# Kernel tuning notes

Measured on AMD Instinct MI355X. Metric: run time of the kernel, lower is better.

Reference implementation:

```python
import jax, jax.numpy as jnp
import numpy as np

V, E, H, F, A, L = 32000, 256, 512, 512, 256, 49  # vocab, embed, hidden, feature, attn, n_locations
B, T = 64, 32


def setup_inputs() -> dict:
    key = jax.random.key(0)
    ks = jax.random.split(key, 16)
    s = lambda k, sh: (jax.random.normal(k, sh, jnp.float32) * 0.02)
    embedding = s(ks[0], (V, E)).at[0].set(0.0)  # padding_idx=0 row zeroed
    return dict(
        image_feats=jax.random.normal(ks[1], (B, L, F), jnp.float32),
        caption_in=jax.random.randint(ks[2], (B, T), 0, V, dtype=jnp.int32),
        embedding=embedding,
        W_init_h=s(ks[3], (F, H)), b_init_h=jnp.zeros((H,), jnp.float32),
        W_init_c=s(ks[4], (F, H)), b_init_c=jnp.zeros((H,), jnp.float32),
        W_feat=s(ks[5], (F, A)), b_feat=jnp.zeros((A,), jnp.float32),
        W_hid=s(ks[6], (H, A)), b_hid=jnp.zeros((A,), jnp.float32),
        W_score=s(ks[7], (A,)), b_score=jnp.zeros((), jnp.float32),
        W_ih=s(ks[8], (E + F, 4 * H)), b_ih=jnp.zeros((4 * H,), jnp.float32),
        W_hh=s(ks[9], (H, 4 * H)), b_hh=jnp.zeros((4 * H,), jnp.float32),
        W_out=s(ks[10], (H, V)), b_out=jnp.zeros((V,), jnp.float32),
    )


def reference(image_feats, caption_in, embedding,
              W_init_h, b_init_h, W_init_c, b_init_c,
              W_feat, b_feat, W_hid, b_hid, W_score, b_score,
              W_ih, b_ih, W_hh, b_hh, W_out, b_out):
    # init_hidden_state: mean over spatial locations -> two linears
    mean_feats = image_feats.mean(axis=1)                      # (B, F)
    h0 = mean_feats @ W_init_h + b_init_h                      # (B, H)
    c0 = mean_feats @ W_init_c + b_init_c                      # (B, H)
    embs = embedding[caption_in]                               # (B, T, E); dropout = identity (eval)
    feat_proj = image_feats @ W_feat + b_feat                  # (B, L, A) - invariant over t, precompute

    def step(carry, emb_t):
        h, c = carry
        # additive attention
        energy = jnp.tanh(feat_proj + (h @ W_hid + b_hid)[:, None, :])   # (B, L, A)
        scores = energy @ W_score + b_score                              # (B, L)
        alpha = jax.nn.softmax(scores, axis=1)                           # (B, L)
        context = jnp.einsum('bl,blf->bf', alpha, image_feats)           # (B, F)
        # LSTMCell (torch gate order i, f, g, o)
        x = jnp.concatenate([emb_t, context], axis=1)                    # (B, E+F)
        gates = x @ W_ih + b_ih + h @ W_hh + b_hh                        # (B, 4H)
        i, f, g, o = jnp.split(gates, 4, axis=1)
        i = jax.nn.sigmoid(i); f = jax.nn.sigmoid(f); o = jax.nn.sigmoid(o)
        c_new = f * c + i * jnp.tanh(g)
        h_new = o * jnp.tanh(c_new)
        logits_t = h_new @ W_out + b_out                                 # (B, V); dropout = identity
        return (h_new, c_new), (logits_t, alpha)

    _, (logits, alphas) = jax.lax.scan(step, (h0, c0), jnp.swapaxes(embs, 0, 1))
    predictions = jnp.swapaxes(logits, 0, 1)   # (B, T, V)
    all_alphas = jnp.swapaxes(alphas, 0, 1)    # (B, T, L)
    return predictions, all_alphas
```

## Files before the change

kernel.cpp:

```cpp
#include <hip/hip_runtime.h>
#include <hip/hip_bf16.h>

typedef _Float16 f16;
typedef _Float16 f16x8 __attribute__((ext_vector_type(8)));
typedef _Float16 f16x4 __attribute__((ext_vector_type(4)));
typedef _Float16 f16x2 __attribute__((ext_vector_type(2)));
typedef float f32x4 __attribute__((ext_vector_type(4)));
typedef unsigned long long ull;

#define B_ 64
#define T_ 32
#define L_ 49
#define F_ 512
#define H_ 512
#define A_ 256
#define E_ 256
#define V_ 32000
#define G4 2048
#define NG 32
#define NLOG 125
#define SLOT 16

#define ALOAD32(p)     __hip_atomic_load((const unsigned*)(p), __ATOMIC_RELAXED, __HIP_MEMORY_SCOPE_AGENT)
#define ASTORE32(p, v) __hip_atomic_store((unsigned*)(p), (v), __ATOMIC_RELAXED, __HIP_MEMORY_SCOPE_AGENT)
#define ASTORE64(p, v) __hip_atomic_store((ull*)(p), (v), __ATOMIC_RELAXED, __HIP_MEMORY_SCOPE_AGENT)
#define AADD(p)        __hip_atomic_fetch_add((unsigned*)(p), 1u, __ATOMIC_RELAXED, __HIP_MEMORY_SCOPE_AGENT)

#if defined(__has_builtin)
#if __has_builtin(__builtin_amdgcn_fdot2)
#define HAS_FDOT2 1
#endif
#endif

#define NB_TC0 (64 * 24)
#define NB_TC1 (64 * 16)
#define NB_TC2 (1000 * 16)
#define NB_TC3 (8 * 16)
#define NB_CVT 1568
#define NB_EMB 2048
#define NB_INIT 64
#define NB_FP  196

__device__ void dev_tcvt(const float* __restrict__ x, f16* __restrict__ y,
                         int R, int C, int bx, int by, char* smem) {
    float (*ls)[33] = (float(*)[33])smem;
    int c0 = bx * 32, r0 = by * 32;
    int tid = threadIdx.x;
    int rr = tid >> 3, cs = (tid & 7) * 4;
    float4 v = *(const float4*)&x[(size_t)(r0 + rr) * C + c0 + cs];
    ls[rr][cs] = v.x; ls[rr][cs + 1] = v.y; ls[rr][cs + 2] = v.z; ls[rr][cs + 3] = v.w;
    __syncthreads();
    int cr = tid >> 3, rs = (tid & 7) * 4;
    f16x4 o = {(f16)ls[rs][cr], (f16)ls[rs + 1][cr], (f16)ls[rs + 2][cr], (f16)ls[rs + 3][cr]};
    *(f16x4*)&y[(size_t)(c0 + cr) * R + r0 + rs] = o;
}

__global__ __launch_bounds__(256) void k_prep(
    const float* __restrict__ image_feats, const int* __restrict__ caption,
    const float* __restrict__ embedding,
    const float* __restrict__ W_init_h, const float* __restrict__ b_init_h,
    const float* __restrict__ W_init_c, const float* __restrict__ b_init_c,
    const float* __restrict__ W_feat, const float* __restrict__ b_feat,
    const float* __restrict__ W_hid, const float* __restrict__ W_ih,
    const float* __restrict__ W_hh, const float* __restrict__ W_out,
    f16* __restrict__ feats16, f16* __restrict__ embs16,
    f16* __restrict__ WihT, f16* __restrict__ WhhT,
    f16* __restrict__ WoutT, f16* __restrict__ WhidT,
    f16* __restrict__ hslab, float* __restrict__ c_cur,
    float* __restrict__ featproj) {
    __shared__ __align__(16) char smem[32768];
    int bid = blockIdx.x, tid = threadIdx.x;
    int r = bid;
    if (r < NB_TC0) { dev_tcvt(W_ih, WihT, E_ + F_, G4, r % 64, r / 64, smem); return; }
    r -= NB_TC0;
    if (r < NB_TC1) { dev_tcvt(W_hh, WhhT, H_, G4, r % 64, r / 64, smem); return; }
    r -= NB_TC1;
    if (r < NB_TC2) { dev_tcvt(W_out, WoutT, H_, V_, r % 1000, r / 1000, smem); return; }
    r -= NB_TC2;
    if (r < NB_TC3) { dev_tcvt(W_hid, WhidT, H_, A_, r % 8, r / 8, smem); return; }
    r -= NB_TC3;
    if (r < NB_CVT) {
        int i = r * 256 + tid;
        float4 v = ((const float4*)image_feats)[i];
        f16x4 h = {(f16)v.x, (f16)v.y, (f16)v.z, (f16)v.w};
        ((f16x4*)feats16)[i] = h;
        return;
    }
    r -= NB_CVT;
    if (r < NB_EMB) {
        int tok = caption[r];
        embs16[(size_t)r * E_ + tid] = (f16)embedding[(size_t)tok * E_ + tid];
        return;
    }
    r -= NB_EMB;
    if (r < NB_INIT) {
        float* mean = (float*)smem;
        int b = r;
        for (int f = tid; f < F_; f += 256) {
            float s = 0.f;
            for (int l = 0; l < L_; ++l) s += image_feats[((size_t)b * L_ + l) * F_ + f];
            mean[f] = s * (1.f / 49.f);
        }
        __syncthreads();
        for (int h = tid; h < H_; h += 256) {
            float a = b_init_h[h], c = b_init_c[h];
            for (int k = 0; k < F_; ++k) {
                float m = mean[k];
                a += m * W_init_h[k * H_ + h];
                c += m * W_init_c[k * H_ + h];
            }
            hslab[(size_t)b * H_ + h] = (f16)a;
            c_cur[b * H_ + h] = c;
        }
        return;
    }
    r -= NB_INIT;
    {
        float (*fs)[F_] = (float(*)[F_])smem;
        int r0 = r * 16;
        for (int i = tid; i < 16 * F_; i += 256)
            fs[i >> 9][i & 511] = image_feats[(size_t)r0 * F_ + i];
        __syncthreads();
        float acc[16];
#pragma unroll
        for (int q = 0; q < 16; ++q) acc[q] = 0.f;
        for (int k = 0; k < F_; ++k) {
            float w = W_feat[k * A_ + tid];
#pragma unroll
            for (int q = 0; q < 16; ++q) acc[q] += fs[q][k] * w;
        }
        float bb = b_feat[tid];
#pragma unroll
        for (int q = 0; q < 16; ++q) featproj[(size_t)(r0 + q) * A_ + tid] = acc[q] + bb;
    }
}

struct Smem128 { f16 As[128][40]; f16 Bs[128][40]; };

__device__ __forceinline__ void gemm128_body1(
    const f16* __restrict__ A, int lda, const f16* __restrict__ Bt, int ldb,
    f16* __restrict__ Cv, int M, int K, int mtiles, int bid,
    const float* __restrict__ bias0, const float* __restrict__ bias1, Smem128* sm) {
    int m0 = (bid % mtiles) * 128, n0 = (bid / mtiles) * 128;
    int tid = threadIdx.x, lane = tid & 63, wave = tid >> 6;
    int wr = (wave >> 1) * 64, wc = (wave & 1) * 64;
    int frow = lane & 15, fk = (lane >> 4) * 8;
    int ra = tid >> 2, ka = (tid & 3) * 8;
    f32x4 acc[4][4];
#pragma unroll
    for (int i = 0; i < 4; ++i)
#pragma unroll
        for (int j = 0; j < 4; ++j) { acc[i][j][0]=0.f; acc[i][j][1]=0.f; acc[i][j][2]=0.f; acc[i][j][3]=0.f; }

    for (int k0 = 0; k0 < K; k0 += 32) {
        f16x8 a0 = *(const f16x8*)&A[(size_t)(m0 + ra) * lda + k0 + ka];
        f16x8 a1 = *(const f16x8*)&A[(size_t)(m0 + 64 + ra) * lda + k0 + ka];
        f16x8 b0 = *(const f16x8*)&Bt[(size_t)(n0 + ra) * ldb + k0 + ka];
        f16x8 b1 = *(const f16x8*)&Bt[(size_t)(n0 + 64 + ra) * ldb + k0 + ka];
        __syncthreads();
        *(f16x8*)&sm->As[ra][ka] = a0;
        *(f16x8*)&sm->As[64 + ra][ka] = a1;
        *(f16x8*)&sm->Bs[ra][ka] = b0;
        *(f16x8*)&sm->Bs[64 + ra][ka] = b1;
        __syncthreads();
        f16x8 av[4], bv[4];
#pragma unroll
        for (int i = 0; i < 4; ++i) {
            av[i] = *(f16x8*)&sm->As[wr + i * 16 + frow][fk];
            bv[i] = *(f16x8*)&sm->Bs[wc + i * 16 + frow][fk];
        }
#pragma unroll
        for (int mi = 0; mi < 4; ++mi)
#pragma unroll
            for (int ni = 0; ni < 4; ++ni)
                acc[mi][ni] = __builtin_amdgcn_mfma_f32_16x16x32_f16(av[mi], bv[ni], acc[mi][ni], 0, 0, 0);
    }
    int rq = (lane >> 4) * 4;
#pragma unroll
    for (int mi = 0; mi < 4; ++mi)
#pragma unroll
        for (int ni = 0; ni < 4; ++ni) {
            int cc = n0 + wc + ni * 16 + frow;
            float badd = (bias0 ? bias0[cc] : 0.f) + (bias1 ? bias1[cc] : 0.f);
#pragma unroll
            for (int r = 0; r < 4; ++r) {
                int rr = m0 + wr + mi * 16 + rq + r;
                if (rr < M)
                    Cv[((size_t)rr * 512 + (cc & 511)) * 4 + (cc >> 9)] =
                        (f16)(acc[mi][ni][r] + badd);
            }
        }
}

__global__ __launch_bounds__(256) void k_gemm_pre(
    int split,
    const f16* A0, int lda0, const f16* B0, int ldb0, f16* C0, int M0, int K0, int mt0,
    const f16* A1, int lda1, const f16* B1, int ldb1, f16* C1, int M1, int K1, int mt1,
    const float* bias0, const float* bias1) {
    __shared__ Smem128 sm;
    int bid = blockIdx.x;
    if (bid < split)
        gemm128_body1(A0, lda0, B0, ldb0, C0, M0, K0, mt0, bid,
                      (const float*)nullptr, (const float*)nullptr, &sm);
    else
        gemm128_body1(A1, lda1, B1, ldb1, C1, M1, K1, mt1, bid - split,
                      bias0, bias1, &sm);
}

struct GateSm {
    float fp[L_][A_];
    float ea[A_];
    float ws[A_];
    float sc[64];
    float alpha[64];
    unsigned hL[256];
};
struct GemmSm {
    f16 w[64][512];
    union {
        f16 hs[64][512];
        f16 hwT16[64][72];
    } u;
};
struct LogSm { f16 hs[64][512]; };

__device__ __forceinline__ void wait_cnt(const unsigned* p, unsigned target) {
    if (threadIdx.x == 0) {
        while (ALOAD32(p) < target) __builtin_amdgcn_s_sleep(1);
    }
    __syncthreads();
    asm volatile("" ::: "memory");
}

__device__ __forceinline__ float sigm(float x) { return 1.f / (1.f + __expf(-x)); }
__device__ __forceinline__ float tanh_f(float x) { return 1.f - 2.f / (1.f + __expf(2.f * x)); }

__global__ __launch_bounds__(256, 1) void k_steps(
    const f16* __restrict__ WhhT, const f16* __restrict__ WhidT,
    const float* __restrict__ featproj, const float* __restrict__ b_hid,
    const float* __restrict__ W_score, const float* __restrict__ b_score,
    const f16* __restrict__ embP, const f16* __restrict__ fp2P,
    const float* __restrict__ c_cur,
    f16* __restrict__ hslab, f16* __restrict__ hwslab,
    const f16* __restrict__ WoutT, const float* __restrict__ b_out,
    float* __restrict__ preds, float* __restrict__ out_alpha,
    unsigned* __restrict__ cntH, unsigned* __restrict__ cntW,
    unsigned* __restrict__ cntH2) {
    __shared__ __align__(16) char smraw[sizeof(GemmSm)];
    int bid = blockIdx.x, tid = threadIdx.x;

    if (bid < 64) {
        int b = bid;
        GateSm* S = (GateSm*)smraw;
        for (int i = tid; i < L_ * A_; i += 256)
            ((float*)S->fp)[i] = featproj[(size_t)b * L_ * A_ + i];
        S->ws[tid] = W_score[tid];
        float bhid_r = b_hid[tid];
        float bsc = b_score[0];
        S->hL[tid] = ((const unsigned*)hslab)[(size_t)b * 256 + tid];
        float cs0 = c_cur[b * H_ + 2 * tid], cs1 = c_cur[b * H_ + 2 * tid + 1];
        const f16* wrow = WhidT + (size_t)tid * 512;
        int wv = tid >> 6, ln = tid & 63;
        __syncthreads();

        for (int t = 0; t < T_; ++t) {
            {
                float acc = bhid_r;
                const f16x8* hL8 = (const f16x8*)S->hL;
#pragma unroll 16
                for (int kk = 0; kk < 64; ++kk) {
                    union { f16x8 v; f16x2 p[4]; } uw, uh;
                    uw.v = *(const f16x8*)&wrow[kk * 8];
                    uh.v = hL8[kk];
#ifdef HAS_FDOT2
                    acc = __builtin_amdgcn_fdot2(uw.p[0], uh.p[0], acc, false);
                    acc = __builtin_amdgcn_fdot2(uw.p[1], uh.p[1], acc, false);
                    acc = __builtin_amdgcn_fdot2(uw.p[2], uh.p[2], acc, false);
                    acc = __builtin_amdgcn_fdot2(uw.p[3], uh.p[3], acc, false);
#else
#pragma unroll
                    for (int e = 0; e < 8; ++e) acc += (float)uw.v[e] * (float)uh.v[e];
#endif
                }
                S->ea[tid] = acc;
            }
            __syncthreads();
            for (int l = wv; l < L_; l += 4) {
                float p = 0.f;
#pragma unroll
                for (int q = 0; q < 4; ++q) {
                    int j = ln + q * 64;
                    p += tanh_f(S->fp[l][j] + S->ea[j]) * S->ws[j];
                }
#pragma unroll
                for (int off = 32; off > 0; off >>= 1) p += __shfl_xor(p, off);
                if (ln == 0) S->sc[l] = p;
            }
            __syncthreads();
            if (tid < 64) {
                float v = (tid < L_) ? S->sc[tid] + bsc : -3.4e38f;
                float m = v;
#pragma unroll
                for (int off = 32; off > 0; off >>= 1) m = fmaxf(m, __shfl_xor(m, off));
                float e = (tid < L_) ? __expf(v - m) : 0.f;
                float s = e;
#pragma unroll
                for (int off = 32; off > 0; off >>= 1) s += __shfl_xor(s, off);
                if (tid < L_) {
                    float al = e / s;
                    S->alpha[tid] = al;
                    out_alpha[((size_t)b * T_ + t) * L_ + tid] = al;
                }
            }
            __syncthreads();
            float s8[8];
#pragma unroll
            for (int i = 0; i < 8; ++i) s8[i] = 0.f;
            {
                const f16* fpb = fp2P + (size_t)b * L_ * G4 + 8 * tid;
#pragma unroll 7
                for (int l = 0; l < L_; ++l) {
                    float a = S->alpha[l];
                    f16x8 fv = *(const f16x8*)&fpb[(size_t)l * G4];
#pragma unroll
                    for (int i = 0; i < 8; ++i) s8[i] += a * (float)fv[i];
                }
            }
            f16x8 ep = *(const f16x8*)&embP[((size_t)b * T_ + t) * G4 + 8 * tid];
            wait_cnt(&cntW[t * SLOT], NG);
            {
                f16x8 hw = *(const f16x8*)&hwslab[((size_t)t * B_ + b) * G4 + 8 * tid];
                float gA[8];
#pragma unroll
                for (int i = 0; i < 8; ++i) gA[i] = (float)hw[i] + (float)ep[i] + s8[i];
                float cn0 = sigm(gA[1]) * cs0 + sigm(gA[0]) * tanh_f(gA[2]);
                float cn1 = sigm(gA[5]) * cs1 + sigm(gA[4]) * tanh_f(gA[6]);
                float hn0 = sigm(gA[3]) * tanh_f(cn0);
                float hn1 = sigm(gA[7]) * tanh_f(cn1);
                cs0 = cn0; cs1 = cn1;
                union { f16 h[2]; unsigned u; } pk;
                pk.h[0] = (f16)hn0; pk.h[1] = (f16)hn1;
                S->hL[tid] = pk.u;
                ASTORE32((unsigned*)hslab + ((size_t)(t + 1) * B_ + b) * 256 + tid, pk.u);
            }
            __syncthreads();
            if (tid == 0) {
                AADD(&cntH[(t + 1) * SLOT]);
                AADD(&cntH2[(t + 1) * SLOT]);
            }
        }
    } else if (bid < 64 + NG) {
        int g = bid - 64;
        GemmSm* S = (GemmSm*)smraw;
        for (int i = 0; i < 16; ++i) {
            int idx = i * 256 + tid;
            int r = idx >> 6, ch = idx & 63;
            int cc = (r & 3) * 512 + 16 * g + (r >> 2);
            *(f16x8*)&S->w[r][(ch ^ (r & 7)) * 8] =
                *(const f16x8*)&WhhT[(size_t)cc * 512 + ch * 8];
        }
        int wvv = tid >> 6, lane = tid & 63;
        int frow = lane & 15, q = lane >> 4, sw = frow & 7, rq = q * 4;
        int bo = tid >> 2, cq = (tid & 3) * 4;
        __syncthreads();

        for (int t = 0; t < T_; ++t) {
            if (t) wait_cnt(&cntH[t * SLOT], 64);
            {
                const f16* hsrc = hslab + (size_t)t * B_ * H_;
#pragma unroll
                for (int i = 0; i < 16; ++i) {
                    int idx = i * 256 + tid;
                    int r = idx >> 6, ch = idx & 63;
                    *(f16x8*)&S->u.hs[r][(ch ^ (r & 7)) * 8] =
                        *(const f16x8*)&hsrc[(size_t)r * H_ + ch * 8];
                }
            }
            __syncthreads();
            f32x4 a4[4];
#pragma unroll
            for (int mi = 0; mi < 4; ++mi) { a4[mi][0]=0.f; a4[mi][1]=0.f; a4[mi][2]=0.f; a4[mi][3]=0.f; }
#pragma unroll
            for (int kk = 0; kk < 16; ++kk) {
                int ch = ((kk * 4 + q) ^ sw) * 8;
                f16x8 bv = *(f16x8*)&S->w[wvv * 16 + frow][ch];
#pragma unroll
                for (int mi = 0; mi < 4; ++mi) {
                    f16x8 av = *(f16x8*)&S->u.hs[mi * 16 + frow][ch];
                    a4[mi] = __builtin_amdgcn_mfma_f32_16x16x32_f16(av, bv, a4[mi], 0, 0, 0);
                }
            }
            __syncthreads();
#pragma unroll
            for (int mi = 0; mi < 4; ++mi)
#pragma unroll
                for (int r = 0; r < 4; ++r)
                    S->u.hwT16[mi * 16 + rq + r][wvv * 16 + frow] = (f16)a4[mi][r];
            __syncthreads();
            {
                f16* dst = hwslab + ((size_t)t * B_ + bo) * G4 + 64 * g + cq;
#pragma unroll
                for (int e = 0; e < 4; ++e) {
                    union { f16 h[4]; ull u; } pk;
                    *(f16x4*)pk.h = *(f16x4*)&S->u.hwT16[bo][cq + 16 * e];
                    ASTORE64(dst + 16 * e, pk.u);
                }
            }
            __syncthreads();
            if (tid == 0) AADD(&cntW[t * SLOT]);
        }
    } else {
        int nt = bid - 64 - NG;
        int n0 = nt * 256;
        LogSm* S = (LogSm*)smraw;
        int wvv = tid >> 6, lane = tid & 63;
        int frow = lane & 15, q = lane >> 4, sw = frow & 7, rq = q * 4;

        for (int t = 0; t < T_; ++t) {
            wait_cnt(&cntH2[(t + 1) * SLOT], 64);
            {
                const f16* hsrc = hslab + (size_t)(t + 1) * B_ * H_;
#pragma unroll
                for (int i = 0; i < 16; ++i) {
                    int idx = i * 256 + tid;
                    int r = idx >> 6, ch = idx & 63;
                    *(f16x8*)&S->hs[r][(ch ^ (r & 7)) * 8] =
                        *(const f16x8*)&hsrc[(size_t)r * H_ + ch * 8];
                }
            }
            __syncthreads();
            f32x4 acc[4][4];
#pragma unroll
            for (int mi = 0; mi < 4; ++mi)
#pragma unroll
                for (int ni = 0; ni < 4; ++ni) { acc[mi][ni][0]=0.f; acc[mi][ni][1]=0.f; acc[mi][ni][2]=0.f; acc[mi][ni][3]=0.f; }
#pragma unroll 4
            for (int kk = 0; kk < 16; ++kk) {
                int ch = ((kk * 4 + q) ^ sw) * 8;
                f16x8 av[4], bv[4];
#pragma unroll
                for (int mi = 0; mi < 4; ++mi)
                    av[mi] = *(f16x8*)&S->hs[mi * 16 + frow][ch];
#pragma unroll
                for (int ni = 0; ni < 4; ++ni)
                    bv[ni] = *(const f16x8*)&WoutT[(size_t)(n0 + wvv * 64 + ni * 16 + frow) * 512 + kk * 32 + q * 8];
#pragma unroll
                for (int mi = 0; mi < 4; ++mi)
#pragma unroll
                    for (int ni = 0; ni < 4; ++ni)
                        acc[mi][ni] = __builtin_amdgcn_mfma_f32_16x16x32_f16(av[mi], bv[ni], acc[mi][ni], 0, 0, 0);
            }
#pragma unroll
            for (int ni = 0; ni < 4; ++ni) {
                int cc = n0 + wvv * 64 + ni * 16 + frow;
                float badd = b_out[cc];
#pragma unroll
                for (int mi = 0; mi < 4; ++mi)
#pragma unroll
                    for (int r = 0; r < 4; ++r) {
                        int b = mi * 16 + rq + r;
                        preds[((size_t)b * T_ + t) * V_ + cc] = acc[mi][ni][r] + badd;
                    }
            }
        }
    }
}

extern "C" void kernel_launch(void* const* d_in, const int* in_sizes, int n_in,
                              void* d_out, int out_size, void* d_ws, size_t ws_size,
                              hipStream_t stream) {
    const float* image_feats = (const float*)d_in[0];
    const int*   caption     = (const int*)d_in[1];
    const float* embedding   = (const float*)d_in[2];
    const float* W_init_h    = (const float*)d_in[3];
    const float* b_init_h    = (const float*)d_in[4];
    const float* W_init_c    = (const float*)d_in[5];
    const float* b_init_c    = (const float*)d_in[6];
    const float* W_feat      = (const float*)d_in[7];
    const float* b_feat      = (const float*)d_in[8];
    const float* W_hid       = (const float*)d_in[9];
    const float* b_hid       = (const float*)d_in[10];
    const float* W_score     = (const float*)d_in[11];
    const float* b_score     = (const float*)d_in[12];
    const float* W_ih        = (const float*)d_in[13];
    const float* b_ih        = (const float*)d_in[14];
    const float* W_hh        = (const float*)d_in[15];
    const float* b_hh        = (const float*)d_in[16];
    const float* W_out       = (const float*)d_in[17];
    const float* b_out       = (const float*)d_in[18];

    float* preds = (float*)d_out;
    float* out_alpha = preds + (size_t)B_ * T_ * V_;

    size_t off = 0;
    char* base = (char*)d_ws;
    auto carve = [&](size_t bytes) {
        void* p = base + off;
        off += (bytes + 255) & ~(size_t)255;
        return p;
    };
    const int MP = 3200;
    f16* fp2P       = (f16*)carve((size_t)MP * G4 * 2);
    f16* embP       = (f16*)carve((size_t)B_ * T_ * G4 * 2);
    float* featproj = (float*)carve((size_t)B_ * L_ * A_ * 4);
    float* c_cur    = (float*)carve((size_t)B_ * H_ * 4);
    f16* hslab      = (f16*)carve((size_t)(T_ + 1) * B_ * H_ * 2);
    f16* hwslab     = (f16*)carve((size_t)T_ * B_ * G4 * 2);
    unsigned* cnts  = (unsigned*)carve(3 * (T_ + 2) * SLOT * 4);
    f16* feats16    = (f16*)carve((size_t)MP * F_ * 2);
    f16* embs16     = (f16*)carve((size_t)B_ * T_ * E_ * 2);
    f16* WihT       = (f16*)carve((size_t)G4 * (E_ + F_) * 2);
    f16* WhhT       = (f16*)carve((size_t)G4 * H_ * 2);
    f16* WoutT      = (f16*)carve((size_t)V_ * H_ * 2);
    f16* WhidT      = (f16*)carve((size_t)A_ * H_ * 2);
    unsigned* cntH  = cnts;
    unsigned* cntW  = cnts + (T_ + 2) * SLOT;
    unsigned* cntH2 = cnts + 2 * (T_ + 2) * SLOT;
    (void)ws_size; (void)in_sizes; (void)n_in; (void)out_size;

    {
        int nb = NB_TC0 + NB_TC1 + NB_TC2 + NB_TC3 + NB_CVT + NB_EMB + NB_INIT + NB_FP;
        hipLaunchKernelGGL(k_prep, dim3(nb), dim3(256), 0, stream,
                           image_feats, caption, embedding,
                           W_init_h, b_init_h, W_init_c, b_init_c,
                           W_feat, b_feat, W_hid, W_ih, W_hh, W_out,
                           feats16, embs16, WihT, WhhT, WoutT, WhidT,
                           hslab, c_cur, featproj);
    }
    hipLaunchKernelGGL(k_gemm_pre, dim3(400 + 256), dim3(256), 0, stream,
                       400,
                       feats16, F_, WihT + E_, E_ + F_, fp2P, B_ * L_, F_, 25,
                       embs16, E_, WihT, E_ + F_, embP, B_ * T_, E_, B_ * T_ / 128,
                       b_ih, b_hh);
    hipMemsetAsync(cnts, 0, 3 * (T_ + 2) * SLOT * 4, stream);
    hipLaunchKernelGGL(k_steps, dim3(64 + NG + NLOG), dim3(256), 0, stream,
                       WhhT, WhidT, featproj, b_hid, W_score, b_score,
                       embP, fp2P, c_cur, hslab, hwslab,
                       WoutT, b_out, preds, out_alpha,
                       cntH, cntW, cntH2);
}
```

Measured before the change: 772.4 us.

## Move LSTM cell update into W_hh slice blocks and batch logits over two steps

The LSTM cell nonlinearity moves from the 64 per-batch attention blocks into the 32 W_hh slice blocks. The attention blocks now publish only the embedding-plus-context gate contribution, and the slice blocks combine it with their fp32 h@W_hh result, keep c in registers and write h directly. This removes one cross-block round-trip per step: previously the hw partials went to global memory, then attention blocks computed h and signalled back. The logits blocks now handle two timesteps per pass (128 rows), which halves the number of W_out reads at the cost of more accumulator registers and a one-step delay before logits for the earlier step start.

```diff
diff --git a/kernel.cpp b/kernel.cpp
--- a/kernel.cpp
+++ b/kernel.cpp
@@ -215,14 +215,14 @@
     float alpha[64];
     unsigned hL[256];
 };
-struct GemmSm {
+struct SliceSm {
     f16 w[64][512];
     union {
         f16 hs[64][512];
-        f16 hwT16[64][72];
+        float hwT[64][68];
     } u;
 };
-struct LogSm { f16 hs[64][512]; };
+struct LogSm { f16 hs[128][512]; };
 
 __device__ __forceinline__ void wait_cnt(const unsigned* p, unsigned target) {
     if (threadIdx.x == 0) {
@@ -241,12 +241,12 @@
     const float* __restrict__ W_score, const float* __restrict__ b_score,
     const f16* __restrict__ embP, const f16* __restrict__ fp2P,
     const float* __restrict__ c_cur,
-    f16* __restrict__ hslab, f16* __restrict__ hwslab,
+    f16* __restrict__ hslab, f16* __restrict__ gsumP,
     const f16* __restrict__ WoutT, const float* __restrict__ b_out,
     float* __restrict__ preds, float* __restrict__ out_alpha,
-    unsigned* __restrict__ cntH, unsigned* __restrict__ cntW,
+    unsigned* __restrict__ cntH, unsigned* __restrict__ cntG,
     unsigned* __restrict__ cntH2) {
-    __shared__ __align__(16) char smraw[sizeof(GemmSm)];
+    __shared__ __align__(16) char smraw[sizeof(LogSm)];
     int bid = blockIdx.x, tid = threadIdx.x;
 
     if (bid < 64) {
@@ -257,13 +257,15 @@
         S->ws[tid] = W_score[tid];
         float bhid_r = b_hid[tid];
         float bsc = b_score[0];
-        S->hL[tid] = ((const unsigned*)hslab)[(size_t)b * 256 + tid];
-        float cs0 = c_cur[b * H_ + 2 * tid], cs1 = c_cur[b * H_ + 2 * tid + 1];
         const f16* wrow = WhidT + (size_t)tid * 512;
+        const unsigned* hsl32 = (const unsigned*)hslab;
         int wv = tid >> 6, ln = tid & 63;
         __syncthreads();
 
         for (int t = 0; t < T_; ++t) {
+            if (t) wait_cnt(&cntH[t * SLOT], NG);
+            S->hL[tid] = hsl32[((size_t)t * B_ + b) * 256 + tid];
+            __syncthreads();
             {
                 float acc = bhid_r;
                 const f16x8* hL8 = (const f16x8*)S->hL;
@@ -313,10 +315,10 @@
                 }
             }
             __syncthreads();
-            float s8[8];
-#pragma unroll
-            for (int i = 0; i < 8; ++i) s8[i] = 0.f;
             {
+                float s8[8];
+#pragma unroll
+                for (int i = 0; i < 8; ++i) s8[i] = 0.f;
                 const f16* fpb = fp2P + (size_t)b * L_ * G4 + 8 * tid;
 #pragma unroll 7
                 for (int l = 0; l < L_; ++l) {
@@ -325,33 +327,20 @@
 #pragma unroll
                     for (int i = 0; i < 8; ++i) s8[i] += a * (float)fv[i];
                 }
-            }
-            f16x8 ep = *(const f16x8*)&embP[((size_t)b * T_ + t) * G4 + 8 * tid];
-            wait_cnt(&cntW[t * SLOT], NG);
-            {
-                f16x8 hw = *(const f16x8*)&hwslab[((size_t)t * B_ + b) * G4 + 8 * tid];
-                float gA[8];
-#pragma unroll
-                for (int i = 0; i < 8; ++i) gA[i] = (float)hw[i] + (float)ep[i] + s8[i];
-                float cn0 = sigm(gA[1]) * cs0 + sigm(gA[0]) * tanh_f(gA[2]);
-                float cn1 = sigm(gA[5]) * cs1 + sigm(gA[4]) * tanh_f(gA[6]);
-                float hn0 = sigm(gA[3]) * tanh_f(cn0);
-                float hn1 = sigm(gA[7]) * tanh_f(cn1);
-                cs0 = cn0; cs1 = cn1;
-                union { f16 h[2]; unsigned u; } pk;
-                pk.h[0] = (f16)hn0; pk.h[1] = (f16)hn1;
-                S->hL[tid] = pk.u;
-                ASTORE32((unsigned*)hslab + ((size_t)(t + 1) * B_ + b) * 256 + tid, pk.u);
-            }
-            __syncthreads();
-            if (tid == 0) {
-                AADD(&cntH[(t + 1) * SLOT]);
-                AADD(&cntH2[(t + 1) * SLOT]);
-            }
+                f16x8 ep = *(const f16x8*)&embP[((size_t)b * T_ + t) * G4 + 8 * tid];
+                union { f16 h[8]; ull u[2]; } pk;
+#pragma unroll
+                for (int i = 0; i < 8; ++i) pk.h[i] = (f16)((float)ep[i] + s8[i]);
+                ull* gdst = (ull*)&gsumP[((size_t)t * B_ + b) * G4 + 8 * tid];
+                ASTORE64(gdst, pk.u[0]);
+                ASTORE64(gdst + 1, pk.u[1]);
+            }
+            __syncthreads();
+            if (tid == 0) AADD(&cntG[t * SLOT]);
         }
     } else if (bid < 64 + NG) {
         int g = bid - 64;
-        GemmSm* S = (GemmSm*)smraw;
+        SliceSm* S = (SliceSm*)smraw;
         for (int i = 0; i < 16; ++i) {
             int idx = i * 256 + tid;
             int r = idx >> 6, ch = idx & 63;
@@ -361,11 +350,15 @@
         }
         int wvv = tid >> 6, lane = tid & 63;
         int frow = lane & 15, q = lane >> 4, sw = frow & 7, rq = q * 4;
-        int bo = tid >> 2, cq = (tid & 3) * 4;
+        int b = tid >> 2, quad = tid & 3;
+        float cr[4];
+#pragma unroll
+        for (int d = 0; d < 4; ++d)
+            cr[d] = c_cur[b * H_ + 16 * g + 4 * quad + d];
         __syncthreads();
 
         for (int t = 0; t < T_; ++t) {
-            if (t) wait_cnt(&cntH[t * SLOT], 64);
+            if (t) wait_cnt(&cntH[t * SLOT], NG);
             {
                 const f16* hsrc = hslab + (size_t)t * B_ * H_;
 #pragma unroll
@@ -390,24 +383,42 @@
                     a4[mi] = __builtin_amdgcn_mfma_f32_16x16x32_f16(av, bv, a4[mi], 0, 0, 0);
                 }
             }
-            __syncthreads();
+            wait_cnt(&cntG[t * SLOT], 64);
 #pragma unroll
             for (int mi = 0; mi < 4; ++mi)
 #pragma unroll
                 for (int r = 0; r < 4; ++r)
-                    S->u.hwT16[mi * 16 + rq + r][wvv * 16 + frow] = (f16)a4[mi][r];
+                    S->u.hwT[mi * 16 + rq + r][wvv * 16 + frow] = a4[mi][r];
             __syncthreads();
             {
-                f16* dst = hwslab + ((size_t)t * B_ + bo) * G4 + 64 * g + cq;
-#pragma unroll
-                for (int e = 0; e < 4; ++e) {
-                    union { f16 h[4]; ull u; } pk;
-                    *(f16x4*)pk.h = *(f16x4*)&S->u.hwT16[bo][cq + 16 * e];
-                    ASTORE64(dst + 16 * e, pk.u);
-                }
-            }
-            __syncthreads();
-            if (tid == 0) AADD(&cntW[t * SLOT]);
+                const f16* gp = &gsumP[((size_t)t * B_ + b) * G4 + 64 * g + 16 * quad];
+                f16x8 q0 = *(const f16x8*)gp;
+                f16x8 q1 = *(const f16x8*)(gp + 8);
+                float gl[16];
+#pragma unroll
+                for (int i = 0; i < 8; ++i) { gl[i] = (float)q0[i]; gl[8 + i] = (float)q1[i]; }
+                const float* hwrow = &S->u.hwT[b][16 * quad];
+                f16 hv[4];
+#pragma unroll
+                for (int d = 0; d < 4; ++d) {
+                    float gi = hwrow[4 * d]     + gl[4 * d];
+                    float gf = hwrow[4 * d + 1] + gl[4 * d + 1];
+                    float gg = hwrow[4 * d + 2] + gl[4 * d + 2];
+                    float go = hwrow[4 * d + 3] + gl[4 * d + 3];
+                    float cn = sigm(gf) * cr[d] + sigm(gi) * tanh_f(gg);
+                    float hn = sigm(go) * tanh_f(cn);
+                    cr[d] = cn;
+                    hv[d] = (f16)hn;
+                }
+                union { f16 h[4]; ull u; } ph;
+                *(f16x4*)ph.h = *(f16x4*)hv;
+                ASTORE64((ull*)&hslab[((size_t)(t + 1) * B_ + b) * H_ + 16 * g + 4 * quad], ph.u);
+            }
+            __syncthreads();
+            if (tid == 0) {
+                AADD(&cntH[(t + 1) * SLOT]);
+                AADD(&cntH2[(t + 1) * SLOT]);
+            }
         }
     } else {
         int nt = bid - 64 - NG;
@@ -416,12 +427,12 @@
         int wvv = tid >> 6, lane = tid & 63;
         int frow = lane & 15, q = lane >> 4, sw = frow & 7, rq = q * 4;
 
-        for (int t = 0; t < T_; ++t) {
-            wait_cnt(&cntH2[(t + 1) * SLOT], 64);
+        for (int tc = 0; tc < T_ / 2; ++tc) {
+            wait_cnt(&cntH2[(2 * tc + 2) * SLOT], NG);
             {
-                const f16* hsrc = hslab + (size_t)(t + 1) * B_ * H_;
-#pragma unroll
-                for (int i = 0; i < 16; ++i) {
+                const f16* hsrc = hslab + (size_t)(2 * tc + 1) * B_ * H_;
+#pragma unroll
+                for (int i = 0; i < 32; ++i) {
                     int idx = i * 256 + tid;
                     int r = idx >> 6, ch = idx & 63;
                     *(f16x8*)&S->hs[r][(ch ^ (r & 7)) * 8] =
@@ -429,23 +440,23 @@
                 }
             }
             __syncthreads();
-            f32x4 acc[4][4];
-#pragma unroll
-            for (int mi = 0; mi < 4; ++mi)
+            f32x4 acc[8][4];
+#pragma unroll
+            for (int mi = 0; mi < 8; ++mi)
 #pragma unroll
                 for (int ni = 0; ni < 4; ++ni) { acc[mi][ni][0]=0.f; acc[mi][ni][1]=0.f; acc[mi][ni][2]=0.f; acc[mi][ni][3]=0.f; }
-#pragma unroll 4
+#pragma unroll 2
             for (int kk = 0; kk < 16; ++kk) {
                 int ch = ((kk * 4 + q) ^ sw) * 8;
-                f16x8 av[4], bv[4];
-#pragma unroll
-                for (int mi = 0; mi < 4; ++mi)
+                f16x8 av[8], bv[4];
+#pragma unroll
+                for (int mi = 0; mi < 8; ++mi)
                     av[mi] = *(f16x8*)&S->hs[mi * 16 + frow][ch];
 #pragma unroll
                 for (int ni = 0; ni < 4; ++ni)
                     bv[ni] = *(const f16x8*)&WoutT[(size_t)(n0 + wvv * 64 + ni * 16 + frow) * 512 + kk * 32 + q * 8];
 #pragma unroll
-                for (int mi = 0; mi < 4; ++mi)
+                for (int mi = 0; mi < 8; ++mi)
 #pragma unroll
                     for (int ni = 0; ni < 4; ++ni)
                         acc[mi][ni] = __builtin_amdgcn_mfma_f32_16x16x32_f16(av[mi], bv[ni], acc[mi][ni], 0, 0, 0);
@@ -455,13 +466,15 @@
                 int cc = n0 + wvv * 64 + ni * 16 + frow;
                 float badd = b_out[cc];
 #pragma unroll
-                for (int mi = 0; mi < 4; ++mi)
+                for (int mi = 0; mi < 8; ++mi)
 #pragma unroll
                     for (int r = 0; r < 4; ++r) {
-                        int b = mi * 16 + rq + r;
-                        preds[((size_t)b * T_ + t) * V_ + cc] = acc[mi][ni][r] + badd;
+                        int rr = mi * 16 + rq + r;
+                        int tt = 2 * tc + (rr >> 6), bb2 = rr & 63;
+                        preds[((size_t)bb2 * T_ + tt) * V_ + cc] = acc[mi][ni][r] + badd;
                     }
             }
+            __syncthreads();
         }
     }
 }
@@ -505,7 +518,7 @@
     float* featproj = (float*)carve((size_t)B_ * L_ * A_ * 4);
     float* c_cur    = (float*)carve((size_t)B_ * H_ * 4);
     f16* hslab      = (f16*)carve((size_t)(T_ + 1) * B_ * H_ * 2);
-    f16* hwslab     = (f16*)carve((size_t)T_ * B_ * G4 * 2);
+    f16* gsumP      = (f16*)carve((size_t)T_ * B_ * G4 * 2);
     unsigned* cnts  = (unsigned*)carve(3 * (T_ + 2) * SLOT * 4);
     f16* feats16    = (f16*)carve((size_t)MP * F_ * 2);
     f16* embs16     = (f16*)carve((size_t)B_ * T_ * E_ * 2);
@@ -514,7 +527,7 @@
     f16* WoutT      = (f16*)carve((size_t)V_ * H_ * 2);
     f16* WhidT      = (f16*)carve((size_t)A_ * H_ * 2);
     unsigned* cntH  = cnts;
-    unsigned* cntW  = cnts + (T_ + 2) * SLOT;
+    unsigned* cntG  = cnts + (T_ + 2) * SLOT;
     unsigned* cntH2 = cnts + 2 * (T_ + 2) * SLOT;
     (void)ws_size; (void)in_sizes; (void)n_in; (void)out_size;
 
@@ -535,7 +548,7 @@
     hipMemsetAsync(cnts, 0, 3 * (T_ + 2) * SLOT * 4, stream);
     hipLaunchKernelGGL(k_steps, dim3(64 + NG + NLOG), dim3(256), 0, stream,
                        WhhT, WhidT, featproj, b_hid, W_score, b_score,
-                       embP, fp2P, c_cur, hslab, hwslab,
+                       embP, fp2P, c_cur, hslab, gsumP,
                        WoutT, b_out, preds, out_alpha,
-                       cntH, cntW, cntH2);
-}
+                       cntH, cntG, cntH2);
+}
```

New measurement: 961.3 us. 24.5% more time.

## Fold h@W_hh into per-batch gate blocks and batch logits over two steps

Applied to the files above, without the earlier changes.

Removes the 32 separate h@W_hh GEMM blocks and their cross-block counter handshakes. Each per-batch gate block now computes its own h@W_hh contribution with fdot2 from a pre-packed, pair-interleaved fp16 copy of W_hh streamed from global/L2. Per-batch flags replace the shared counters, and the logits blocks now process two time steps (128 rows) per W_out tile load, halving W_out reloads. The trade is that every gate block reads 2 MB of W_hh per step on the serial critical path, and logits output is delayed by one extra step.

```diff
diff --git a/kernel.cpp b/kernel.cpp
--- a/kernel.cpp
+++ b/kernel.cpp
@@ -17,14 +17,11 @@
 #define E_ 256
 #define V_ 32000
 #define G4 2048
-#define NG 32
 #define NLOG 125
 #define SLOT 16
 
 #define ALOAD32(p)     __hip_atomic_load((const unsigned*)(p), __ATOMIC_RELAXED, __HIP_MEMORY_SCOPE_AGENT)
 #define ASTORE32(p, v) __hip_atomic_store((unsigned*)(p), (v), __ATOMIC_RELAXED, __HIP_MEMORY_SCOPE_AGENT)
-#define ASTORE64(p, v) __hip_atomic_store((ull*)(p), (v), __ATOMIC_RELAXED, __HIP_MEMORY_SCOPE_AGENT)
-#define AADD(p)        __hip_atomic_fetch_add((unsigned*)(p), 1u, __ATOMIC_RELAXED, __HIP_MEMORY_SCOPE_AGENT)
 
 #if defined(__has_builtin)
 #if __has_builtin(__builtin_amdgcn_fdot2)
@@ -33,7 +30,7 @@
 #endif
 
 #define NB_TC0 (64 * 24)
-#define NB_TC1 (64 * 16)
+#define NB_WHH 256
 #define NB_TC2 (1000 * 16)
 #define NB_TC3 (8 * 16)
 #define NB_CVT 1568
@@ -64,7 +61,7 @@
     const float* __restrict__ W_hid, const float* __restrict__ W_ih,
     const float* __restrict__ W_hh, const float* __restrict__ W_out,
     f16* __restrict__ feats16, f16* __restrict__ embs16,
-    f16* __restrict__ WihT, f16* __restrict__ WhhT,
+    f16* __restrict__ WihT, f16* __restrict__ WhhPp,
     f16* __restrict__ WoutT, f16* __restrict__ WhidT,
     f16* __restrict__ hslab, float* __restrict__ c_cur,
     float* __restrict__ featproj) {
@@ -73,8 +70,24 @@
     int r = bid;
     if (r < NB_TC0) { dev_tcvt(W_ih, WihT, E_ + F_, G4, r % 64, r / 64, smem); return; }
     r -= NB_TC0;
-    if (r < NB_TC1) { dev_tcvt(W_hh, WhhT, H_, G4, r % 64, r / 64, smem); return; }
-    r -= NB_TC1;
+    if (r < NB_WHH) {
+        int k2 = r;
+        const float* r0 = W_hh + (size_t)(2 * k2) * G4;
+        const float* r1 = W_hh + (size_t)(2 * k2 + 1) * G4;
+        f16 buf[16];
+#pragma unroll
+        for (int j = 0; j < 8; ++j) {
+            int pc = 8 * tid + j;
+            int c = (pc >> 2) + (pc & 3) * 512;
+            buf[2 * j]     = (f16)r0[c];
+            buf[2 * j + 1] = (f16)r1[c];
+        }
+        f16* dst = WhhPp + ((size_t)k2 * G4 + 8 * tid) * 2;
+        *(f16x8*)dst = *(f16x8*)buf;
+        *(f16x8*)(dst + 8) = *(f16x8*)(buf + 8);
+        return;
+    }
+    r -= NB_WHH;
     if (r < NB_TC2) { dev_tcvt(W_out, WoutT, H_, V_, r % 1000, r / 1000, smem); return; }
     r -= NB_TC2;
     if (r < NB_TC3) { dev_tcvt(W_hid, WhidT, H_, A_, r % 8, r / 8, smem); return; }
@@ -213,22 +226,16 @@
     float ws[A_];
     float sc[64];
     float alpha[64];
-    unsigned hL[256];
+    __align__(16) unsigned hL[256];
 };
-struct GemmSm {
-    f16 w[64][512];
-    union {
-        f16 hs[64][512];
-        f16 hwT16[64][72];
-    } u;
-};
-struct LogSm { f16 hs[64][512]; };
-
-__device__ __forceinline__ void wait_cnt(const unsigned* p, unsigned target) {
-    if (threadIdx.x == 0) {
+struct LogSm { f16 hs[128][512]; };
+
+__device__ __forceinline__ void wait_n(const unsigned* flags, int n, unsigned target) {
+    int l = threadIdx.x & 63;
+    if (l < n) {
+        const unsigned* p = flags + l * SLOT;
         while (ALOAD32(p) < target) __builtin_amdgcn_s_sleep(1);
     }
-    __syncthreads();
     asm volatile("" ::: "memory");
 }
 
@@ -236,17 +243,16 @@
 __device__ __forceinline__ float tanh_f(float x) { return 1.f - 2.f / (1.f + __expf(2.f * x)); }
 
 __global__ __launch_bounds__(256, 1) void k_steps(
-    const f16* __restrict__ WhhT, const f16* __restrict__ WhidT,
+    const f16* __restrict__ WhhPp, const f16* __restrict__ WhidT,
     const float* __restrict__ featproj, const float* __restrict__ b_hid,
     const float* __restrict__ W_score, const float* __restrict__ b_score,
     const f16* __restrict__ embP, const f16* __restrict__ fp2P,
     const float* __restrict__ c_cur,
-    f16* __restrict__ hslab, f16* __restrict__ hwslab,
+    f16* __restrict__ hslab,
     const f16* __restrict__ WoutT, const float* __restrict__ b_out,
     float* __restrict__ preds, float* __restrict__ out_alpha,
-    unsigned* __restrict__ cntH, unsigned* __restrict__ cntW,
-    unsigned* __restrict__ cntH2) {
-    __shared__ __align__(16) char smraw[sizeof(GemmSm)];
+    unsigned* __restrict__ gateflag) {
+    __shared__ __align__(16) char smraw[sizeof(LogSm)];
     int bid = blockIdx.x, tid = threadIdx.x;
 
     if (bid < 64) {
@@ -260,6 +266,7 @@
         S->hL[tid] = ((const unsigned*)hslab)[(size_t)b * 256 + tid];
         float cs0 = c_cur[b * H_ + 2 * tid], cs1 = c_cur[b * H_ + 2 * tid + 1];
         const f16* wrow = WhidT + (size_t)tid * 512;
+        const f16* wbase = WhhPp + (size_t)16 * tid;
         int wv = tid >> 6, ln = tid & 63;
         __syncthreads();
 
@@ -326,13 +333,48 @@
                     for (int i = 0; i < 8; ++i) s8[i] += a * (float)fv[i];
                 }
             }
+            float acc8[8];
+#pragma unroll
+            for (int i = 0; i < 8; ++i) acc8[i] = 0.f;
+            {
+                const uint4* hq = (const uint4*)S->hL;
+#pragma unroll 2
+                for (int kq = 0; kq < 64; ++kq) {
+                    uint4 hu = hq[kq];
+                    const f16* wp = wbase + (size_t)kq * 4 * 4096;
+                    unsigned hs4[4] = {hu.x, hu.y, hu.z, hu.w};
+#pragma unroll
+                    for (int j = 0; j < 4; ++j) {
+                        union { unsigned u; f16x2 v; } hk; hk.u = hs4[j];
+                        union { f16x8 v; f16x2 p[4]; } w0, w1;
+                        w0.v = *(const f16x8*)(wp + j * 4096);
+                        w1.v = *(const f16x8*)(wp + j * 4096 + 8);
+#ifdef HAS_FDOT2
+                        acc8[0] = __builtin_amdgcn_fdot2(w0.p[0], hk.v, acc8[0], false);
+                        acc8[1] = __builtin_amdgcn_fdot2(w0.p[1], hk.v, acc8[1], false);
+                        acc8[2] = __builtin_amdgcn_fdot2(w0.p[2], hk.v, acc8[2], false);
+                        acc8[3] = __builtin_amdgcn_fdot2(w0.p[3], hk.v, acc8[3], false);
+                        acc8[4] = __builtin_amdgcn_fdot2(w1.p[0], hk.v, acc8[4], false);
+                        acc8[5] = __builtin_amdgcn_fdot2(w1.p[1], hk.v, acc8[5], false);
+                        acc8[6] = __builtin_amdgcn_fdot2(w1.p[2], hk.v, acc8[6], false);
+                        acc8[7] = __builtin_amdgcn_fdot2(w1.p[3], hk.v, acc8[7], false);
+#else
+                        float h0 = (float)hk.v.x, h1 = (float)hk.v.y;
+#pragma unroll
+                        for (int i = 0; i < 4; ++i) {
+                            acc8[i]     += h0 * (float)w0.p[i].x + h1 * (float)w0.p[i].y;
+                            acc8[4 + i] += h0 * (float)w1.p[i].x + h1 * (float)w1.p[i].y;
+                        }
+#endif
+                    }
+                }
+            }
             f16x8 ep = *(const f16x8*)&embP[((size_t)b * T_ + t) * G4 + 8 * tid];
-            wait_cnt(&cntW[t * SLOT], NG);
+            __syncthreads();
             {
-                f16x8 hw = *(const f16x8*)&hwslab[((size_t)t * B_ + b) * G4 + 8 * tid];
                 float gA[8];
 #pragma unroll
-                for (int i = 0; i < 8; ++i) gA[i] = (float)hw[i] + (float)ep[i] + s8[i];
+                for (int i = 0; i < 8; ++i) gA[i] = acc8[i] + (float)ep[i] + s8[i];
                 float cn0 = sigm(gA[1]) * cs0 + sigm(gA[0]) * tanh_f(gA[2]);
                 float cn1 = sigm(gA[5]) * cs1 + sigm(gA[4]) * tanh_f(gA[6]);
                 float hn0 = sigm(gA[3]) * tanh_f(cn0);
@@ -344,84 +386,22 @@
                 ASTORE32((unsigned*)hslab + ((size_t)(t + 1) * B_ + b) * 256 + tid, pk.u);
             }
             __syncthreads();
-            if (tid == 0) {
-                AADD(&cntH[(t + 1) * SLOT]);
-                AADD(&cntH2[(t + 1) * SLOT]);
-            }
-        }
-    } else if (bid < 64 + NG) {
-        int g = bid - 64;
-        GemmSm* S = (GemmSm*)smraw;
-        for (int i = 0; i < 16; ++i) {
-            int idx = i * 256 + tid;
-            int r = idx >> 6, ch = idx & 63;
-            int cc = (r & 3) * 512 + 16 * g + (r >> 2);
-            *(f16x8*)&S->w[r][(ch ^ (r & 7)) * 8] =
-                *(const f16x8*)&WhhT[(size_t)cc * 512 + ch * 8];
-        }
-        int wvv = tid >> 6, lane = tid & 63;
-        int frow = lane & 15, q = lane >> 4, sw = frow & 7, rq = q * 4;
-        int bo = tid >> 2, cq = (tid & 3) * 4;
-        __syncthreads();
-
-        for (int t = 0; t < T_; ++t) {
-            if (t) wait_cnt(&cntH[t * SLOT], 64);
-            {
-                const f16* hsrc = hslab + (size_t)t * B_ * H_;
-#pragma unroll
-                for (int i = 0; i < 16; ++i) {
-                    int idx = i * 256 + tid;
-                    int r = idx >> 6, ch = idx & 63;
-                    *(f16x8*)&S->u.hs[r][(ch ^ (r & 7)) * 8] =
-                        *(const f16x8*)&hsrc[(size_t)r * H_ + ch * 8];
-                }
-            }
-            __syncthreads();
-            f32x4 a4[4];
-#pragma unroll
-            for (int mi = 0; mi < 4; ++mi) { a4[mi][0]=0.f; a4[mi][1]=0.f; a4[mi][2]=0.f; a4[mi][3]=0.f; }
-#pragma unroll
-            for (int kk = 0; kk < 16; ++kk) {
-                int ch = ((kk * 4 + q) ^ sw) * 8;
-                f16x8 bv = *(f16x8*)&S->w[wvv * 16 + frow][ch];
-#pragma unroll
-                for (int mi = 0; mi < 4; ++mi) {
-                    f16x8 av = *(f16x8*)&S->u.hs[mi * 16 + frow][ch];
-                    a4[mi] = __builtin_amdgcn_mfma_f32_16x16x32_f16(av, bv, a4[mi], 0, 0, 0);
-                }
-            }
-            __syncthreads();
-#pragma unroll
-            for (int mi = 0; mi < 4; ++mi)
-#pragma unroll
-                for (int r = 0; r < 4; ++r)
-                    S->u.hwT16[mi * 16 + rq + r][wvv * 16 + frow] = (f16)a4[mi][r];
-            __syncthreads();
-            {
-                f16* dst = hwslab + ((size_t)t * B_ + bo) * G4 + 64 * g + cq;
-#pragma unroll
-                for (int e = 0; e < 4; ++e) {
-                    union { f16 h[4]; ull u; } pk;
-                    *(f16x4*)pk.h = *(f16x4*)&S->u.hwT16[bo][cq + 16 * e];
-                    ASTORE64(dst + 16 * e, pk.u);
-                }
-            }
-            __syncthreads();
-            if (tid == 0) AADD(&cntW[t * SLOT]);
+            if (tid == 0) ASTORE32(&gateflag[b * SLOT], (unsigned)(t + 2));
         }
     } else {
-        int nt = bid - 64 - NG;
+        int nt = bid - 64;
         int n0 = nt * 256;
         LogSm* S = (LogSm*)smraw;
         int wvv = tid >> 6, lane = tid & 63;
         int frow = lane & 15, q = lane >> 4, sw = frow & 7, rq = q * 4;
 
-        for (int t = 0; t < T_; ++t) {
-            wait_cnt(&cntH2[(t + 1) * SLOT], 64);
+        for (int tc = 0; tc < T_ / 2; ++tc) {
+            wait_n(gateflag, 64, (unsigned)(2 * tc + 3));
+            __syncthreads();
             {
-                const f16* hsrc = hslab + (size_t)(t + 1) * B_ * H_;
-#pragma unroll
-                for (int i = 0; i < 16; ++i) {
+                const f16* hsrc = hslab + (size_t)(2 * tc + 1) * B_ * H_;
+#pragma unroll
+                for (int i = 0; i < 32; ++i) {
                     int idx = i * 256 + tid;
                     int r = idx >> 6, ch = idx & 63;
                     *(f16x8*)&S->hs[r][(ch ^ (r & 7)) * 8] =
@@ -429,23 +409,23 @@
                 }
             }
             __syncthreads();
-            f32x4 acc[4][4];
-#pragma unroll
-            for (int mi = 0; mi < 4; ++mi)
+            f32x4 acc[8][4];
+#pragma unroll
+            for (int mi = 0; mi < 8; ++mi)
 #pragma unroll
                 for (int ni = 0; ni < 4; ++ni) { acc[mi][ni][0]=0.f; acc[mi][ni][1]=0.f; acc[mi][ni][2]=0.f; acc[mi][ni][3]=0.f; }
-#pragma unroll 4
+#pragma unroll 2
             for (int kk = 0; kk < 16; ++kk) {
                 int ch = ((kk * 4 + q) ^ sw) * 8;
-                f16x8 av[4], bv[4];
-#pragma unroll
-                for (int mi = 0; mi < 4; ++mi)
+                f16x8 av[8], bv[4];
+#pragma unroll
+                for (int mi = 0; mi < 8; ++mi)
                     av[mi] = *(f16x8*)&S->hs[mi * 16 + frow][ch];
 #pragma unroll
                 for (int ni = 0; ni < 4; ++ni)
                     bv[ni] = *(const f16x8*)&WoutT[(size_t)(n0 + wvv * 64 + ni * 16 + frow) * 512 + kk * 32 + q * 8];
 #pragma unroll
-                for (int mi = 0; mi < 4; ++mi)
+                for (int mi = 0; mi < 8; ++mi)
 #pragma unroll
                     for (int ni = 0; ni < 4; ++ni)
                         acc[mi][ni] = __builtin_amdgcn_mfma_f32_16x16x32_f16(av[mi], bv[ni], acc[mi][ni], 0, 0, 0);
@@ -455,13 +435,15 @@
                 int cc = n0 + wvv * 64 + ni * 16 + frow;
                 float badd = b_out[cc];
 #pragma unroll
-                for (int mi = 0; mi < 4; ++mi)
+                for (int mi = 0; mi < 8; ++mi)
 #pragma unroll
                     for (int r = 0; r < 4; ++r) {
-                        int b = mi * 16 + rq + r;
-                        preds[((size_t)b * T_ + t) * V_ + cc] = acc[mi][ni][r] + badd;
+                        int rr = mi * 16 + rq + r;
+                        int tt = 2 * tc + (rr >> 6), bb2 = rr & 63;
+                        preds[((size_t)bb2 * T_ + tt) * V_ + cc] = acc[mi][ni][r] + badd;
                     }
             }
+            __syncthreads();
         }
     }
 }
@@ -505,26 +487,22 @@
     float* featproj = (float*)carve((size_t)B_ * L_ * A_ * 4);
     float* c_cur    = (float*)carve((size_t)B_ * H_ * 4);
     f16* hslab      = (f16*)carve((size_t)(T_ + 1) * B_ * H_ * 2);
-    f16* hwslab     = (f16*)carve((size_t)T_ * B_ * G4 * 2);
-    unsigned* cnts  = (unsigned*)carve(3 * (T_ + 2) * SLOT * 4);
+    unsigned* flags = (unsigned*)carve(64 * SLOT * 4);
     f16* feats16    = (f16*)carve((size_t)MP * F_ * 2);
     f16* embs16     = (f16*)carve((size_t)B_ * T_ * E_ * 2);
     f16* WihT       = (f16*)carve((size_t)G4 * (E_ + F_) * 2);
-    f16* WhhT       = (f16*)carve((size_t)G4 * H_ * 2);
+    f16* WhhPp      = (f16*)carve((size_t)256 * G4 * 2 * 2);
     f16* WoutT      = (f16*)carve((size_t)V_ * H_ * 2);
     f16* WhidT      = (f16*)carve((size_t)A_ * H_ * 2);
-    unsigned* cntH  = cnts;
-    unsigned* cntW  = cnts + (T_ + 2) * SLOT;
-    unsigned* cntH2 = cnts + 2 * (T_ + 2) * SLOT;
     (void)ws_size; (void)in_sizes; (void)n_in; (void)out_size;
 
     {
-        int nb = NB_TC0 + NB_TC1 + NB_TC2 + NB_TC3 + NB_CVT + NB_EMB + NB_INIT + NB_FP;
+        int nb = NB_TC0 + NB_WHH + NB_TC2 + NB_TC3 + NB_CVT + NB_EMB + NB_INIT + NB_FP;
         hipLaunchKernelGGL(k_prep, dim3(nb), dim3(256), 0, stream,
                            image_feats, caption, embedding,
                            W_init_h, b_init_h, W_init_c, b_init_c,
                            W_feat, b_feat, W_hid, W_ih, W_hh, W_out,
-                           feats16, embs16, WihT, WhhT, WoutT, WhidT,
+                           feats16, embs16, WihT, WhhPp, WoutT, WhidT,
                            hslab, c_cur, featproj);
     }
     hipLaunchKernelGGL(k_gemm_pre, dim3(400 + 256), dim3(256), 0, stream,
@@ -532,10 +510,9 @@
                        feats16, F_, WihT + E_, E_ + F_, fp2P, B_ * L_, F_, 25,
                        embs16, E_, WihT, E_ + F_, embP, B_ * T_, E_, B_ * T_ / 128,
                        b_ih, b_hh);
-    hipMemsetAsync(cnts, 0, 3 * (T_ + 2) * SLOT * 4, stream);
-    hipLaunchKernelGGL(k_steps, dim3(64 + NG + NLOG), dim3(256), 0, stream,
-                       WhhT, WhidT, featproj, b_hid, W_score, b_score,
-                       embP, fp2P, c_cur, hslab, hwslab,
-                       WoutT, b_out, preds, out_alpha,
-                       cntH, cntW, cntH2);
-}
+    hipMemsetAsync(flags, 0, 64 * SLOT * 4, stream);
+    hipLaunchKernelGGL(k_steps, dim3(64 + NLOG), dim3(256), 0, stream,
+                       WhhPp, WhidT, featproj, b_hid, W_score, b_score,
+                       embP, fp2P, c_cur, hslab,
+                       WoutT, b_out, preds, out_alpha, flags);
+}
```

Result: slower. 1.256 ms (+62.6%).

## Replace atomic counters with per-block flags and batch logits over two timesteps

Applied to the files above, without the earlier changes.

Per-step atomic-add counters are replaced with per-block monotonic flags that waiters poll in parallel, one thread per producer, which removes contention on a single shared counter. The logits blocks now process two timesteps per iteration (128 rows), so each W_out tile is streamed once per two steps instead of every step. The cost is double the shared memory for the h tile, more accumulator registers, and logits for even steps being delayed until the following step finishes.

```diff
diff --git a/kernel.cpp b/kernel.cpp
--- a/kernel.cpp
+++ b/kernel.cpp
@@ -24,7 +24,6 @@
 #define ALOAD32(p)     __hip_atomic_load((const unsigned*)(p), __ATOMIC_RELAXED, __HIP_MEMORY_SCOPE_AGENT)
 #define ASTORE32(p, v) __hip_atomic_store((unsigned*)(p), (v), __ATOMIC_RELAXED, __HIP_MEMORY_SCOPE_AGENT)
 #define ASTORE64(p, v) __hip_atomic_store((ull*)(p), (v), __ATOMIC_RELAXED, __HIP_MEMORY_SCOPE_AGENT)
-#define AADD(p)        __hip_atomic_fetch_add((unsigned*)(p), 1u, __ATOMIC_RELAXED, __HIP_MEMORY_SCOPE_AGENT)
 
 #if defined(__has_builtin)
 #if __has_builtin(__builtin_amdgcn_fdot2)
@@ -222,14 +221,16 @@
         f16 hwT16[64][72];
     } u;
 };
-struct LogSm { f16 hs[64][512]; };
-
-__device__ __forceinline__ void wait_cnt(const unsigned* p, unsigned target) {
-    if (threadIdx.x == 0) {
+struct LogSm { f16 hs[128][512]; };
+
+__device__ __forceinline__ void wait_n(const unsigned* flags, int n, unsigned target) {
+    int tid = threadIdx.x;
+    if (tid < n) {
+        const unsigned* p = flags + tid * SLOT;
         while (ALOAD32(p) < target) __builtin_amdgcn_s_sleep(1);
     }
+    asm volatile("" ::: "memory");
     __syncthreads();
-    asm volatile("" ::: "memory");
 }
 
 __device__ __forceinline__ float sigm(float x) { return 1.f / (1.f + __expf(-x)); }
@@ -244,9 +245,8 @@
     f16* __restrict__ hslab, f16* __restrict__ hwslab,
     const f16* __restrict__ WoutT, const float* __restrict__ b_out,
     float* __restrict__ preds, float* __restrict__ out_alpha,
-    unsigned* __restrict__ cntH, unsigned* __restrict__ cntW,
-    unsigned* __restrict__ cntH2) {
-    __shared__ __align__(16) char smraw[sizeof(GemmSm)];
+    unsigned* __restrict__ gateflag, unsigned* __restrict__ gemmflag) {
+    __shared__ __align__(16) char smraw[sizeof(LogSm)];
     int bid = blockIdx.x, tid = threadIdx.x;
 
     if (bid < 64) {
@@ -327,7 +327,7 @@
                 }
             }
             f16x8 ep = *(const f16x8*)&embP[((size_t)b * T_ + t) * G4 + 8 * tid];
-            wait_cnt(&cntW[t * SLOT], NG);
+            wait_n(gemmflag, NG, (unsigned)(t + 1));
             {
                 f16x8 hw = *(const f16x8*)&hwslab[((size_t)t * B_ + b) * G4 + 8 * tid];
                 float gA[8];
@@ -344,10 +344,8 @@
                 ASTORE32((unsigned*)hslab + ((size_t)(t + 1) * B_ + b) * 256 + tid, pk.u);
             }
             __syncthreads();
-            if (tid == 0) {
-                AADD(&cntH[(t + 1) * SLOT]);
-                AADD(&cntH2[(t + 1) * SLOT]);
-            }
+            if (tid == 0)
+                ASTORE32(&gateflag[b * SLOT], (unsigned)(t + 2));
         }
     } else if (bid < 64 + NG) {
         int g = bid - 64;
@@ -365,7 +363,7 @@
         __syncthreads();
 
         for (int t = 0; t < T_; ++t) {
-            if (t) wait_cnt(&cntH[t * SLOT], 64);
+            if (t) wait_n(gateflag, 64, (unsigned)(t + 1));
             {
                 const f16* hsrc = hslab + (size_t)t * B_ * H_;
 #pragma unroll
@@ -407,7 +405,8 @@
                 }
             }
             __syncthreads();
-            if (tid == 0) AADD(&cntW[t * SLOT]);
+            if (tid == 0)
+                ASTORE32(&gemmflag[g * SLOT], (unsigned)(t + 1));
         }
     } else {
         int nt = bid - 64 - NG;
@@ -416,12 +415,12 @@
         int wvv = tid >> 6, lane = tid & 63;
         int frow = lane & 15, q = lane >> 4, sw = frow & 7, rq = q * 4;
 
-        for (int t = 0; t < T_; ++t) {
-            wait_cnt(&cntH2[(t + 1) * SLOT], 64);
+        for (int tc = 0; tc < T_ / 2; ++tc) {
+            wait_n(gateflag, 64, (unsigned)(2 * tc + 3));
             {
-                const f16* hsrc = hslab + (size_t)(t + 1) * B_ * H_;
-#pragma unroll
-                for (int i = 0; i < 16; ++i) {
+                const f16* hsrc = hslab + (size_t)(2 * tc + 1) * B_ * H_;
+#pragma unroll
+                for (int i = 0; i < 32; ++i) {
                     int idx = i * 256 + tid;
                     int r = idx >> 6, ch = idx & 63;
                     *(f16x8*)&S->hs[r][(ch ^ (r & 7)) * 8] =
@@ -429,23 +428,23 @@
                 }
             }
             __syncthreads();
-            f32x4 acc[4][4];
-#pragma unroll
-            for (int mi = 0; mi < 4; ++mi)
+            f32x4 acc[8][4];
+#pragma unroll
+            for (int mi = 0; mi < 8; ++mi)
 #pragma unroll
                 for (int ni = 0; ni < 4; ++ni) { acc[mi][ni][0]=0.f; acc[mi][ni][1]=0.f; acc[mi][ni][2]=0.f; acc[mi][ni][3]=0.f; }
-#pragma unroll 4
+#pragma unroll 2
             for (int kk = 0; kk < 16; ++kk) {
                 int ch = ((kk * 4 + q) ^ sw) * 8;
-                f16x8 av[4], bv[4];
-#pragma unroll
-                for (int mi = 0; mi < 4; ++mi)
+                f16x8 av[8], bv[4];
+#pragma unroll
+                for (int mi = 0; mi < 8; ++mi)
                     av[mi] = *(f16x8*)&S->hs[mi * 16 + frow][ch];
 #pragma unroll
                 for (int ni = 0; ni < 4; ++ni)
                     bv[ni] = *(const f16x8*)&WoutT[(size_t)(n0 + wvv * 64 + ni * 16 + frow) * 512 + kk * 32 + q * 8];
 #pragma unroll
-                for (int mi = 0; mi < 4; ++mi)
+                for (int mi = 0; mi < 8; ++mi)
 #pragma unroll
                     for (int ni = 0; ni < 4; ++ni)
                         acc[mi][ni] = __builtin_amdgcn_mfma_f32_16x16x32_f16(av[mi], bv[ni], acc[mi][ni], 0, 0, 0);
@@ -455,13 +454,15 @@
                 int cc = n0 + wvv * 64 + ni * 16 + frow;
                 float badd = b_out[cc];
 #pragma unroll
-                for (int mi = 0; mi < 4; ++mi)
+                for (int mi = 0; mi < 8; ++mi)
 #pragma unroll
                     for (int r = 0; r < 4; ++r) {
-                        int b = mi * 16 + rq + r;
-                        preds[((size_t)b * T_ + t) * V_ + cc] = acc[mi][ni][r] + badd;
+                        int rr = mi * 16 + rq + r;
+                        int tt = 2 * tc + (rr >> 6), bb2 = rr & 63;
+                        preds[((size_t)bb2 * T_ + tt) * V_ + cc] = acc[mi][ni][r] + badd;
                     }
             }
+            __syncthreads();
         }
     }
 }
@@ -506,16 +507,15 @@
     float* c_cur    = (float*)carve((size_t)B_ * H_ * 4);
     f16* hslab      = (f16*)carve((size_t)(T_ + 1) * B_ * H_ * 2);
     f16* hwslab     = (f16*)carve((size_t)T_ * B_ * G4 * 2);
-    unsigned* cnts  = (unsigned*)carve(3 * (T_ + 2) * SLOT * 4);
+    unsigned* flags = (unsigned*)carve((64 + NG) * SLOT * 4);
     f16* feats16    = (f16*)carve((size_t)MP * F_ * 2);
     f16* embs16     = (f16*)carve((size_t)B_ * T_ * E_ * 2);
     f16* WihT       = (f16*)carve((size_t)G4 * (E_ + F_) * 2);
     f16* WhhT       = (f16*)carve((size_t)G4 * H_ * 2);
     f16* WoutT      = (f16*)carve((size_t)V_ * H_ * 2);
     f16* WhidT      = (f16*)carve((size_t)A_ * H_ * 2);
-    unsigned* cntH  = cnts;
-    unsigned* cntW  = cnts + (T_ + 2) * SLOT;
-    unsigned* cntH2 = cnts + 2 * (T_ + 2) * SLOT;
+    unsigned* gateflag = flags;
+    unsigned* gemmflag = flags + 64 * SLOT;
     (void)ws_size; (void)in_sizes; (void)n_in; (void)out_size;
 
     {
@@ -532,10 +532,10 @@
                        feats16, F_, WihT + E_, E_ + F_, fp2P, B_ * L_, F_, 25,
                        embs16, E_, WihT, E_ + F_, embP, B_ * T_, E_, B_ * T_ / 128,
                        b_ih, b_hh);
-    hipMemsetAsync(cnts, 0, 3 * (T_ + 2) * SLOT * 4, stream);
+    hipMemsetAsync(flags, 0, (64 + NG) * SLOT * 4, stream);
     hipLaunchKernelGGL(k_steps, dim3(64 + NG + NLOG), dim3(256), 0, stream,
                        WhhT, WhidT, featproj, b_hid, W_score, b_score,
                        embP, fp2P, c_cur, hslab, hwslab,
                        WoutT, b_out, preds, out_alpha,
-                       cntH, cntW, cntH2);
-}
+                       gateflag, gemmflag);
+}
```

Measured after the change: 728.9 us. 5.6% less time.
